# Performance work log

Measured on AMD Instinct MI355X. Metric: run time of the kernel, lower is better.

Reference implementation:

```python
import jax, jax.numpy as jnp
import numpy as np

D_IN = 1024
D_OUT = 1024
NUM_HEADS = 16
HEAD_DIM = D_OUT // NUM_HEADS


def setup_inputs() -> dict:
    key = jax.random.key(0)
    k_x, k_q, k_k, k_v, k_o = jax.random.split(key, 5)
    # Xavier-uniform-ish init for weights (stored as [d_in, d_out] for x @ W)
    lim = float(np.sqrt(6.0 / (D_IN + D_OUT)) / np.sqrt(2.0))
    lim_o = float(np.sqrt(6.0 / (D_OUT + D_OUT)))
    return {
        "x": jax.random.normal(k_x, (2, 2048, D_IN), dtype=jnp.float32),
        "W_query": jax.random.uniform(k_q, (D_IN, D_OUT), jnp.float32, -lim, lim),
        "W_key": jax.random.uniform(k_k, (D_IN, D_OUT), jnp.float32, -lim, lim),
        "W_value": jax.random.uniform(k_v, (D_IN, D_OUT), jnp.float32, -lim, lim),
        "W_out": jax.random.uniform(k_o, (D_OUT, D_OUT), jnp.float32, -lim_o, lim_o),
        "b_out": jnp.zeros((D_OUT,), dtype=jnp.float32),
    }


def reference(x, W_query, W_key, W_value, W_out, b_out):
    B, S, _ = x.shape
    scale = 1.0 / np.sqrt(HEAD_DIM)

    def split_heads(t):  # [B,S,D] -> [B,H,S,hd]
        return t.reshape(B, S, NUM_HEADS, HEAD_DIM).transpose(0, 2, 1, 3)

    q = split_heads(x @ W_query)
    k = split_heads(x @ W_key)
    v = split_heads(x @ W_value)

    scores = jnp.einsum("bhqd,bhkd->bhqk", q, k) * scale  # [B,H,S,S]
    causal = jnp.tril(jnp.ones((S, S), dtype=bool))  # True = keep
    scores = jnp.where(causal, scores, -jnp.inf)
    weights = jax.nn.softmax(scores, axis=-1)
    ctx = jnp.einsum("bhqk,bhkd->bhqd", weights, v)
    ctx = ctx.transpose(0, 2, 1, 3).reshape(B, S, D_OUT)
    return ctx @ W_out + b_out
```

## Files before the change

### kernel.cpp

```cpp
#include <hip/hip_runtime.h>
#include <hip/hip_bf16.h>


typedef __bf16 bf16_t;
typedef __bf16 bf16x4 __attribute__((ext_vector_type(4)));
typedef __bf16 bf16x8 __attribute__((ext_vector_type(8)));
typedef float f32x4 __attribute__((ext_vector_type(4)));

#define AS_GLOBAL __attribute__((address_space(1)))
#define AS_LDS    __attribute__((address_space(3)))

__device__ __forceinline__ void barrier_lgkm() {
    asm volatile("s_waitcnt lgkmcnt(0)\n\ts_barrier" ::: "memory");
}

__device__ __forceinline__ bf16x8 cvt_bf8(float4 lo, float4 hi) {
    bf16x8 r;
    r[0] = (bf16_t)lo.x; r[1] = (bf16_t)lo.y; r[2] = (bf16_t)lo.z; r[3] = (bf16_t)lo.w;
    r[4] = (bf16_t)hi.x; r[5] = (bf16_t)hi.y; r[6] = (bf16_t)hi.z; r[7] = (bf16_t)hi.w;
    return r;
}

__global__ __launch_bounds__(256) void transpose_cvt4(
    const float* __restrict__ W0, const float* __restrict__ W1,
    const float* __restrict__ W2, const float* __restrict__ W3,
    bf16_t* __restrict__ outbase) {
    __shared__ bf16_t T[64][65];
    int t = threadIdx.x;
    int k0 = blockIdx.x * 64, n0 = blockIdx.y * 64, z = blockIdx.z;
    const float* W = (z == 0) ? W0 : (z == 1) ? W1 : (z == 2) ? W2 : W3;
    bf16_t* WT = outbase + (size_t)z * 1048576;
#pragma unroll
    for (int c = 0; c < 4; c++) {
        int idx = c * 256 + t;
        int row = idx >> 4;
        int col4 = (idx & 15) * 4;
        float4 v = *(const float4*)(W + (k0 + row) * 1024 + n0 + col4);
        T[row][col4 + 0] = (bf16_t)v.x;
        T[row][col4 + 1] = (bf16_t)v.y;
        T[row][col4 + 2] = (bf16_t)v.z;
        T[row][col4 + 3] = (bf16_t)v.w;
    }
    __syncthreads();
#pragma unroll
    for (int c = 0; c < 4; c++) {
        int idx = c * 256 + t;
        int nrow = idx >> 4;
        int kc4 = (idx & 15) * 4;
        bf16x4 o;
        o[0] = T[kc4 + 0][nrow];
        o[1] = T[kc4 + 1][nrow];
        o[2] = T[kc4 + 2][nrow];
        o[3] = T[kc4 + 3][nrow];
        *(bf16x4*)(WT + (n0 + nrow) * 1024 + k0 + kc4) = o;
    }
}

__global__ __launch_bounds__(256) void qkv_gemm(
    const float* __restrict__ X,
    const bf16_t* __restrict__ WqT, const bf16_t* __restrict__ WkT,
    const bf16_t* __restrict__ WvT,
    bf16_t* __restrict__ Qo, bf16_t* __restrict__ Ko, bf16_t* __restrict__ Vo) {
    const int KD = 1024;
    __shared__ __align__(16) bf16_t As[2][4096];
    __shared__ __align__(16) bf16_t Bs[2][4096];
    int tid = threadIdx.x;
    int wave = tid >> 6, lane = tid & 63;
    int quad = lane >> 4, l16 = lane & 15;
    int wm = wave >> 1, wn = wave & 1;
    int z = blockIdx.z;
    const bf16_t* BT = (z == 0) ? WqT : (z == 1) ? WkT : WvT;
    int m0 = blockIdx.x * 128;
    int n0 = blockIdx.y * 128;

    int r = tid >> 2;
    int c8 = (((tid & 3) ^ ((tid >> 3) & 3))) * 8;
    const float*  gA0 = X + (size_t)(m0 + r) * KD + c8;
    const float*  gA1 = X + (size_t)(m0 + 64 + r) * KD + c8;
    const bf16_t* gB0 = BT + (size_t)(n0 + r) * KD + c8;
    const bf16_t* gB1 = BT + (size_t)(n0 + 64 + r) * KD + c8;

    f32x4 acc[4][4];
#pragma unroll
    for (int i = 0; i < 4; i++)
#pragma unroll
        for (int j = 0; j < 4; j++) acc[i][j] = (f32x4){0.f, 0.f, 0.f, 0.f};

    float4 fa0l = *(const float4*)gA0, fa0h = *(const float4*)(gA0 + 4);
    float4 fa1l = *(const float4*)gA1, fa1h = *(const float4*)(gA1 + 4);
    int4 sb0 = *(const int4*)gB0, sb1 = *(const int4*)gB1;
    *(bf16x8*)(As[0] + tid * 8) = cvt_bf8(fa0l, fa0h);
    *(bf16x8*)(As[0] + 2048 + tid * 8) = cvt_bf8(fa1l, fa1h);
    *(int4*)(Bs[0] + tid * 8) = sb0;
    *(int4*)(Bs[0] + 2048 + tid * 8) = sb1;
    fa0l = *(const float4*)(gA0 + 32); fa0h = *(const float4*)(gA0 + 36);
    fa1l = *(const float4*)(gA1 + 32); fa1h = *(const float4*)(gA1 + 36);
    sb0 = *(const int4*)(gB0 + 32); sb1 = *(const int4*)(gB1 + 32);

    int csw = (quad ^ ((l16 >> 1) & 3)) * 8;
#pragma unroll 1
    for (int kk = 0; kk < 32; kk += 2) {
        barrier_lgkm();
        bf16x8 af[4], bfr[4];
#pragma unroll
        for (int mt = 0; mt < 4; mt++)
            af[mt] = *(const bf16x8*)(As[0] + (wm * 64 + mt * 16 + l16) * 32 + csw);
#pragma unroll
        for (int nt = 0; nt < 4; nt++)
            bfr[nt] = *(const bf16x8*)(Bs[0] + (wn * 64 + nt * 16 + l16) * 32 + csw);
        *(bf16x8*)(As[1] + tid * 8) = cvt_bf8(fa0l, fa0h);
        *(bf16x8*)(As[1] + 2048 + tid * 8) = cvt_bf8(fa1l, fa1h);
        *(int4*)(Bs[1] + tid * 8) = sb0;
        *(int4*)(Bs[1] + 2048 + tid * 8) = sb1;
        if (kk + 2 < 32) {
            int k0 = (kk + 2) * 32;
            fa0l = *(const float4*)(gA0 + k0); fa0h = *(const float4*)(gA0 + k0 + 4);
            fa1l = *(const float4*)(gA1 + k0); fa1h = *(const float4*)(gA1 + k0 + 4);
            sb0 = *(const int4*)(gB0 + k0); sb1 = *(const int4*)(gB1 + k0);
        }
        if (z == 2) {
#pragma unroll
            for (int mt = 0; mt < 4; mt++)
#pragma unroll
                for (int nt = 0; nt < 4; nt++)
                    acc[mt][nt] = __builtin_amdgcn_mfma_f32_16x16x32_bf16(
                        bfr[nt], af[mt], acc[mt][nt], 0, 0, 0);
        } else {
#pragma unroll
            for (int mt = 0; mt < 4; mt++)
#pragma unroll
                for (int nt = 0; nt < 4; nt++)
                    acc[mt][nt] = __builtin_amdgcn_mfma_f32_16x16x32_bf16(
                        af[mt], bfr[nt], acc[mt][nt], 0, 0, 0);
        }
        barrier_lgkm();
#pragma unroll
        for (int mt = 0; mt < 4; mt++)
            af[mt] = *(const bf16x8*)(As[1] + (wm * 64 + mt * 16 + l16) * 32 + csw);
#pragma unroll
        for (int nt = 0; nt < 4; nt++)
            bfr[nt] = *(const bf16x8*)(Bs[1] + (wn * 64 + nt * 16 + l16) * 32 + csw);
        if (kk + 2 < 32) {
            *(bf16x8*)(As[0] + tid * 8) = cvt_bf8(fa0l, fa0h);
            *(bf16x8*)(As[0] + 2048 + tid * 8) = cvt_bf8(fa1l, fa1h);
            *(int4*)(Bs[0] + tid * 8) = sb0;
            *(int4*)(Bs[0] + 2048 + tid * 8) = sb1;
            if (kk + 3 < 32) {
                int k0 = (kk + 3) * 32;
                fa0l = *(const float4*)(gA0 + k0); fa0h = *(const float4*)(gA0 + k0 + 4);
                fa1l = *(const float4*)(gA1 + k0); fa1h = *(const float4*)(gA1 + k0 + 4);
                sb0 = *(const int4*)(gB0 + k0); sb1 = *(const int4*)(gB1 + k0);
            }
        }
        if (z == 2) {
#pragma unroll
            for (int mt = 0; mt < 4; mt++)
#pragma unroll
                for (int nt = 0; nt < 4; nt++)
                    acc[mt][nt] = __builtin_amdgcn_mfma_f32_16x16x32_bf16(
                        bfr[nt], af[mt], acc[mt][nt], 0, 0, 0);
        } else {
#pragma unroll
            for (int mt = 0; mt < 4; mt++)
#pragma unroll
                for (int nt = 0; nt < 4; nt++)
                    acc[mt][nt] = __builtin_amdgcn_mfma_f32_16x16x32_bf16(
                        af[mt], bfr[nt], acc[mt][nt], 0, 0, 0);
        }
    }

    if (z == 0) {
#pragma unroll
        for (int mt = 0; mt < 4; mt++) {
            int mg_base = m0 + wm * 64 + mt * 16 + quad * 4;
#pragma unroll
            for (int nt = 0; nt < 4; nt++) {
                int ng = n0 + wn * 64 + nt * 16 + l16;
                int h = ng >> 6, d = ng & 63;
#pragma unroll
                for (int rr = 0; rr < 4; rr++) {
                    int mg = mg_base + rr;
                    int b = mg >> 11, s = mg & 2047;
                    Qo[(((size_t)(b * 16 + h) * 2048) + s) * 64 + d] =
                        (bf16_t)acc[mt][nt][rr];
                }
            }
        }
    } else if (z == 1) {
#pragma unroll
        for (int mt = 0; mt < 4; mt++) {
            int mg_base = m0 + wm * 64 + mt * 16 + quad * 4;
#pragma unroll
            for (int nt = 0; nt < 4; nt++) {
                int ng = n0 + wn * 64 + nt * 16 + l16;
                int h = ng >> 6, dd = ng & 63;
#pragma unroll
                for (int rr = 0; rr < 4; rr++) {
                    int mg = mg_base + rr;
                    int b = mg >> 11, sl = mg & 2047;
                    int kt = sl >> 6, row = sl & 63;
                    int cc = (dd >> 3) ^ (row & 7);
                    Ko[(size_t)(b * 16 + h) * 131072 + kt * 4096 + row * 64 +
                       cc * 8 + (dd & 7)] = (bf16_t)acc[mt][nt][rr];
                }
            }
        }
    } else {
#pragma unroll
        for (int mt = 0; mt < 4; mt++) {
            int sg = m0 + wm * 64 + mt * 16 + l16;
            int b = sg >> 11, sl = sg & 2047;
            int kt = sl >> 6, srow = sl & 63;
#pragma unroll
            for (int nt = 0; nt < 4; nt++) {
                int dg_base = n0 + wn * 64 + nt * 16 + quad * 4;
#pragma unroll
                for (int rr = 0; rr < 4; rr++) {
                    int dg = dg_base + rr;
                    int h = dg >> 6, dd = dg & 63;
                    int cc = (srow >> 3) ^ (dd & 7);
                    Vo[(size_t)(b * 16 + h) * 131072 + kt * 4096 + dd * 64 +
                       cc * 8 + (srow & 7)] = (bf16_t)acc[mt][nt][rr];
                }
            }
        }
    }
}

__device__ __forceinline__ float exp_pwrite(f32x4 sc[4], bf16_t* Ps,
                                            int wave, int quad, int l16) {
    float part = 0.f;
    int rowbase = (wave * 16 + l16) * 64;
    int gran = (quad & 1) * 4;
    int chi = quad >> 1;
#pragma unroll
    for (int nt = 0; nt < 4; nt++) {
        f32x4 p;
#pragma unroll
        for (int rr = 0; rr < 4; rr++) {
            p[rr] = __builtin_amdgcn_exp2f(sc[nt][rr]);
            part += p[rr];
        }
        bf16x4 pb;
#pragma unroll
        for (int rr = 0; rr < 4; rr++) pb[rr] = (bf16_t)p[rr];
        int cc = (nt * 2 + chi) ^ (l16 & 7);
        *(bf16x4*)(Ps + rowbase + cc * 8 + gran) = pb;
    }
    part += __shfl_xor(part, 16);
    part += __shfl_xor(part, 32);
    return part;
}

__global__ __launch_bounds__(256) void attn(
    const bf16_t* __restrict__ Q, const bf16_t* __restrict__ Kt,
    const bf16_t* __restrict__ Vt, bf16_t* __restrict__ ctx) {
    const int S = 2048;
    __shared__ __align__(16) bf16_t Ks[2][4096];
    __shared__ __align__(16) bf16_t Vs[2][4096];
    __shared__ __align__(16) bf16_t Ps[2][4096];
    int tid = threadIdx.x, wave = tid >> 6, lane = tid & 63;
    int quad = lane >> 4, l16 = lane & 15;

    int f = blockIdx.x + 32 * blockIdx.y;
    int g = f >> 8, s = f & 255;
    int qtj = g ? (15 - (s & 15)) : (s & 15);
    int bh = (s >> 4) + 16 * g;
    int h = bh & 15, b = bh >> 4;
    int q0 = qtj * 128;

    const bf16_t* Qbh = Q + (size_t)bh * S * 64;
    const bf16_t* Kbh = Kt + (size_t)bh * 131072;
    const bf16_t* Vbh = Vt + (size_t)bh * 131072;

    const float qs = 0.125f * 1.44269504f;
    bf16x8 aQ[2][2];
#pragma unroll
    for (int sub = 0; sub < 2; sub++) {
        const bf16_t* rq = Qbh + (size_t)(q0 + sub * 64 + wave * 16 + l16) * 64;
#pragma unroll
        for (int ks = 0; ks < 2; ks++) {
            bf16x8 t = *(const bf16x8*)(rq + ks * 32 + quad * 8);
#pragma unroll
            for (int j = 0; j < 8; j++) t[j] = (bf16_t)((float)t[j] * qs);
            aQ[sub][ks] = t;
        }
    }

    float L[2] = {0.f, 0.f};
    f32x4 O[2][4];
#pragma unroll
    for (int sub = 0; sub < 2; sub++)
#pragma unroll
        for (int i = 0; i < 4; i++) O[sub][i] = (f32x4){0.f, 0.f, 0.f, 0.f};

    int tmax = 2 * qtj + 2;
    int4 ska = *(const int4*)(Kbh + tid * 8);
    int4 skb = *(const int4*)(Kbh + 2048 + tid * 8);
    int4 sva = *(const int4*)(Vbh + tid * 8);
    int4 svb = *(const int4*)(Vbh + 2048 + tid * 8);
    *(int4*)(Ks[0] + tid * 8) = ska; *(int4*)(Ks[0] + 2048 + tid * 8) = skb;
    *(int4*)(Vs[0] + tid * 8) = sva; *(int4*)(Vs[0] + 2048 + tid * 8) = svb;
    ska = *(const int4*)(Kbh + 4096 + tid * 8);
    skb = *(const int4*)(Kbh + 6144 + tid * 8);
    sva = *(const int4*)(Vbh + 4096 + tid * 8);
    svb = *(const int4*)(Vbh + 6144 + tid * 8);

#pragma unroll 1
    for (int kt = 0; kt < tmax; kt++) {
        int cur = kt & 1;
        barrier_lgkm();
        bf16x8 kf[4][2], vf[4][2];
#pragma unroll
        for (int nt = 0; nt < 4; nt++) {
            const bf16_t* krow = Ks[cur] + (nt * 16 + l16) * 64;
            const bf16_t* vrow = Vs[cur] + (nt * 16 + l16) * 64;
#pragma unroll
            for (int ks = 0; ks < 2; ks++) {
                int csw = ((ks * 4 + quad) ^ (l16 & 7)) * 8;
                kf[nt][ks] = *(const bf16x8*)(krow + csw);
                vf[nt][ks] = *(const bf16x8*)(vrow + csw);
            }
        }
        if (kt + 1 < tmax) {
            *(int4*)(Ks[cur ^ 1] + tid * 8) = ska;
            *(int4*)(Ks[cur ^ 1] + 2048 + tid * 8) = skb;
            *(int4*)(Vs[cur ^ 1] + tid * 8) = sva;
            *(int4*)(Vs[cur ^ 1] + 2048 + tid * 8) = svb;
        }
        if (kt + 2 < tmax) {
            const bf16_t* kg = Kbh + (kt + 2) * 4096;
            const bf16_t* vg = Vbh + (kt + 2) * 4096;
            ska = *(const int4*)(kg + tid * 8);
            skb = *(const int4*)(kg + 2048 + tid * 8);
            sva = *(const int4*)(vg + tid * 8);
            svb = *(const int4*)(vg + 2048 + tid * 8);
        }

        bool do_lo = (kt < tmax - 1);
        if (do_lo) {
            f32x4 sc[4];
#pragma unroll
            for (int nt = 0; nt < 4; nt++) {
                f32x4 ss = (f32x4){0.f, 0.f, 0.f, 0.f};
                ss = __builtin_amdgcn_mfma_f32_16x16x32_bf16(kf[nt][0], aQ[0][0], ss, 0, 0, 0);
                ss = __builtin_amdgcn_mfma_f32_16x16x32_bf16(kf[nt][1], aQ[0][1], ss, 0, 0, 0);
                sc[nt] = ss;
            }
            if (kt == tmax - 2) {
                int qg = q0 + wave * 16 + l16;
#pragma unroll
                for (int nt = 0; nt < 4; nt++)
#pragma unroll
                    for (int rr = 0; rr < 4; rr++)
                        if (kt * 64 + nt * 16 + quad * 4 + rr > qg) sc[nt][rr] = -1e30f;
            }
            L[0] += exp_pwrite(sc, Ps[0], wave, quad, l16);
        }
        {
            f32x4 sc[4];
#pragma unroll
            for (int nt = 0; nt < 4; nt++) {
                f32x4 ss = (f32x4){0.f, 0.f, 0.f, 0.f};
                ss = __builtin_amdgcn_mfma_f32_16x16x32_bf16(kf[nt][0], aQ[1][0], ss, 0, 0, 0);
                ss = __builtin_amdgcn_mfma_f32_16x16x32_bf16(kf[nt][1], aQ[1][1], ss, 0, 0, 0);
                sc[nt] = ss;
            }
            if (kt == tmax - 1) {
                int qg = q0 + 64 + wave * 16 + l16;
#pragma unroll
                for (int nt = 0; nt < 4; nt++)
#pragma unroll
                    for (int rr = 0; rr < 4; rr++)
                        if (kt * 64 + nt * 16 + quad * 4 + rr > qg) sc[nt][rr] = -1e30f;
            }
            L[1] += exp_pwrite(sc, Ps[1], wave, quad, l16);
        }

#pragma unroll
        for (int ks = 0; ks < 2; ks++) {
            int csw = ((ks * 4 + quad) ^ (l16 & 7)) * 8;
            bf16x8 aPhi = *(const bf16x8*)(Ps[1] + (wave * 16 + l16) * 64 + csw);
            bf16x8 aPlo;
            if (do_lo) aPlo = *(const bf16x8*)(Ps[0] + (wave * 16 + l16) * 64 + csw);
#pragma unroll
            for (int nt = 0; nt < 4; nt++) {
                O[1][nt] = __builtin_amdgcn_mfma_f32_16x16x32_bf16(aPhi, vf[nt][ks],
                                                                   O[1][nt], 0, 0, 0);
                if (do_lo)
                    O[0][nt] = __builtin_amdgcn_mfma_f32_16x16x32_bf16(aPlo, vf[nt][ks],
                                                                       O[0][nt], 0, 0, 0);
            }
        }
    }

#pragma unroll
    for (int sub = 0; sub < 2; sub++) {
        float il[4];
#pragma unroll
        for (int rr = 0; rr < 4; rr++) il[rr] = 1.f / __shfl(L[sub], quad * 4 + rr);
#pragma unroll
        for (int nt = 0; nt < 4; nt++) {
#pragma unroll
            for (int rr = 0; rr < 4; rr++) {
                int qoff = q0 + sub * 64 + wave * 16 + quad * 4 + rr;
                int col = h * 64 + nt * 16 + l16;
                ctx[(size_t)(b * 2048 + qoff) * 1024 + col] =
                    (bf16_t)(O[sub][nt][rr] * il[rr]);
            }
        }
    }
}

__global__ __launch_bounds__(256) void out_gemm(
    const bf16_t* __restrict__ A, const bf16_t* __restrict__ BT,
    const float* __restrict__ bias, float* __restrict__ Cout) {
    const int KD = 1024;
    __shared__ __align__(16) bf16_t As[2][2048];
    __shared__ __align__(16) bf16_t Bs[2][4096];
    int tid = threadIdx.x;
    int wave = tid >> 6, lane = tid & 63;
    int quad = lane >> 4, l16 = lane & 15;
    int wm = wave >> 1, wn = wave & 1;
    int m0 = blockIdx.x * 64;
    int n0 = blockIdx.y * 128;

    int r = tid >> 2;
    int c8 = (((tid & 3) ^ ((tid >> 3) & 3))) * 8;
    const bf16_t* gA  = A + (size_t)(m0 + r) * KD + c8;
    const bf16_t* gB0 = BT + (size_t)(n0 + r) * KD + c8;
    const bf16_t* gB1 = BT + (size_t)(n0 + 64 + r) * KD + c8;

    f32x4 acc[2][4];
#pragma unroll
    for (int i = 0; i < 2; i++)
#pragma unroll
        for (int j = 0; j < 4; j++) acc[i][j] = (f32x4){0.f, 0.f, 0.f, 0.f};

    int4 sa = *(const int4*)gA;
    int4 sb0 = *(const int4*)gB0, sb1 = *(const int4*)gB1;
    *(int4*)(As[0] + tid * 8) = sa;
    *(int4*)(Bs[0] + tid * 8) = sb0;
    *(int4*)(Bs[0] + 2048 + tid * 8) = sb1;
    sa = *(const int4*)(gA + 32);
    sb0 = *(const int4*)(gB0 + 32); sb1 = *(const int4*)(gB1 + 32);

    int csw = (quad ^ ((l16 >> 1) & 3)) * 8;
#pragma unroll 1
    for (int kk = 0; kk < 32; kk += 2) {
        barrier_lgkm();
        bf16x8 af[2], bfr[4];
#pragma unroll
        for (int mt = 0; mt < 2; mt++)
            af[mt] = *(const bf16x8*)(As[0] + (wm * 32 + mt * 16 + l16) * 32 + csw);
#pragma unroll
        for (int nt = 0; nt < 4; nt++)
            bfr[nt] = *(const bf16x8*)(Bs[0] + (wn * 64 + nt * 16 + l16) * 32 + csw);
        *(int4*)(As[1] + tid * 8) = sa;
        *(int4*)(Bs[1] + tid * 8) = sb0;
        *(int4*)(Bs[1] + 2048 + tid * 8) = sb1;
        if (kk + 2 < 32) {
            int k0 = (kk + 2) * 32;
            sa = *(const int4*)(gA + k0);
            sb0 = *(const int4*)(gB0 + k0); sb1 = *(const int4*)(gB1 + k0);
        }
#pragma unroll
        for (int mt = 0; mt < 2; mt++)
#pragma unroll
            for (int nt = 0; nt < 4; nt++)
                acc[mt][nt] = __builtin_amdgcn_mfma_f32_16x16x32_bf16(af[mt], bfr[nt],
                                                                      acc[mt][nt], 0, 0, 0);
        barrier_lgkm();
#pragma unroll
        for (int mt = 0; mt < 2; mt++)
            af[mt] = *(const bf16x8*)(As[1] + (wm * 32 + mt * 16 + l16) * 32 + csw);
#pragma unroll
        for (int nt = 0; nt < 4; nt++)
            bfr[nt] = *(const bf16x8*)(Bs[1] + (wn * 64 + nt * 16 + l16) * 32 + csw);
        if (kk + 2 < 32) {
            *(int4*)(As[0] + tid * 8) = sa;
            *(int4*)(Bs[0] + tid * 8) = sb0;
            *(int4*)(Bs[0] + 2048 + tid * 8) = sb1;
            if (kk + 3 < 32) {
                int k0 = (kk + 3) * 32;
                sa = *(const int4*)(gA + k0);
                sb0 = *(const int4*)(gB0 + k0); sb1 = *(const int4*)(gB1 + k0);
            }
        }
#pragma unroll
        for (int mt = 0; mt < 2; mt++)
#pragma unroll
            for (int nt = 0; nt < 4; nt++)
                acc[mt][nt] = __builtin_amdgcn_mfma_f32_16x16x32_bf16(af[mt], bfr[nt],
                                                                      acc[mt][nt], 0, 0, 0);
    }

#pragma unroll
    for (int mt = 0; mt < 2; mt++) {
        int mg_base = m0 + wm * 32 + mt * 16 + quad * 4;
#pragma unroll
        for (int nt = 0; nt < 4; nt++) {
            int ng = n0 + wn * 64 + nt * 16 + l16;
            float bv = bias[ng];
#pragma unroll
            for (int rr = 0; rr < 4; rr++) {
                int mg = mg_base + rr;
                Cout[(size_t)mg * 1024 + ng] = acc[mt][nt][rr] + bv;
            }
        }
    }
}

extern "C" void kernel_launch(void* const* d_in, const int* in_sizes, int n_in,
                              void* d_out, int out_size, void* d_ws, size_t ws_size,
                              hipStream_t stream) {
    const float* x  = (const float*)d_in[0];
    const float* Wq = (const float*)d_in[1];
    const float* Wk = (const float*)d_in[2];
    const float* Wv = (const float*)d_in[3];
    const float* Wo = (const float*)d_in[4];
    const float* bo = (const float*)d_in[5];
    float* out = (float*)d_out;
    char* ws = (char*)d_ws;

    bf16_t* WTs  = (bf16_t*)(ws + (8u << 20));
    bf16_t* WqT  = WTs;
    bf16_t* WkT  = WTs + 1048576;
    bf16_t* WvT  = WTs + 2097152;
    bf16_t* WoT  = WTs + 3145728;
    bf16_t* Qb   = (bf16_t*)(ws + (16u << 20));
    bf16_t* Kb   = (bf16_t*)(ws + (24u << 20));
    bf16_t* Vb   = (bf16_t*)(ws + (32u << 20));
    bf16_t* ctxb = (bf16_t*)(ws + (40u << 20));

    transpose_cvt4<<<dim3(16, 16, 4), 256, 0, stream>>>(Wq, Wk, Wv, Wo, WTs);
    qkv_gemm<<<dim3(32, 8, 3), 256, 0, stream>>>(x, WqT, WkT, WvT, Qb, Kb, Vb);
    attn<<<dim3(32, 16), 256, 0, stream>>>(Qb, Kb, Vb, ctxb);
    out_gemm<<<dim3(64, 8), 256, 0, stream>>>(ctxb, WoT, bo, out);
}
```

Baseline: 186.9 us.

## Fuse all stages into one cooperative persistent megakernel with grid syncs

```diff
diff --git a/kernel.cpp b/kernel.cpp
--- a/kernel.cpp
+++ b/kernel.cpp
@@ -1,27 +1,566 @@
 #include <hip/hip_runtime.h>
 #include <hip/hip_bf16.h>
-
+#include <hip/hip_cooperative_groups.h>
+
+
+namespace cg = cooperative_groups;
 
 typedef __bf16 bf16_t;
 typedef __bf16 bf16x4 __attribute__((ext_vector_type(4)));
 typedef __bf16 bf16x8 __attribute__((ext_vector_type(8)));
 typedef float f32x4 __attribute__((ext_vector_type(4)));
 
-#define AS_GLOBAL __attribute__((address_space(1)))
-#define AS_LDS    __attribute__((address_space(3)))
+__device__ int g_j1, g_j2;
 
 __device__ __forceinline__ void barrier_lgkm() {
     asm volatile("s_waitcnt lgkmcnt(0)\n\ts_barrier" ::: "memory");
 }
 
-__device__ __forceinline__ bf16x8 cvt_bf8(float4 lo, float4 hi) {
-    bf16x8 r;
-    r[0] = (bf16_t)lo.x; r[1] = (bf16_t)lo.y; r[2] = (bf16_t)lo.z; r[3] = (bf16_t)lo.w;
-    r[4] = (bf16_t)hi.x; r[5] = (bf16_t)hi.y; r[6] = (bf16_t)hi.z; r[7] = (bf16_t)hi.w;
-    return r;
-}
-
-__global__ __launch_bounds__(256) void transpose_cvt4(
+__device__ __forceinline__ float exp_pwrite(f32x4 sc[4], bf16_t* Ps,
+                                            int wave, int quad, int l16) {
+    float part = 0.f;
+    int rowbase = (wave * 16 + l16) * 64;
+    int gran = (quad & 1) * 4;
+    int chi = quad >> 1;
+#pragma unroll
+    for (int nt = 0; nt < 4; nt++) {
+        f32x4 p;
+#pragma unroll
+        for (int rr = 0; rr < 4; rr++) {
+            p[rr] = __builtin_amdgcn_exp2f(sc[nt][rr]);
+            part += p[rr];
+        }
+        bf16x4 pb;
+#pragma unroll
+        for (int rr = 0; rr < 4; rr++) pb[rr] = (bf16_t)p[rr];
+        int cc = (nt * 2 + chi) ^ (l16 & 7);
+        *(bf16x4*)(Ps + rowbase + cc * 8 + gran) = pb;
+    }
+    part += __shfl_xor(part, 16);
+    part += __shfl_xor(part, 32);
+    return part;
+}
+
+
+__device__ __forceinline__ void qkv_body(
+    int mb, int nb, int z, const bf16_t* xb, const bf16_t* WqT,
+    const bf16_t* WkT, const bf16_t* WvT, bf16_t* Qb, bf16_t* Kb, bf16_t* Vb,
+    bf16_t* As, bf16_t* Bs, int tid, int wave, int quad, int l16) {
+    const int KD = 1024;
+    const bf16_t* BT = (z == 0) ? WqT : (z == 1) ? WkT : WvT;
+    int m0 = mb * 128, n0 = nb * 128;
+    int wm = wave >> 1, wn = wave & 1;
+    int r = tid >> 2;
+    int c8 = (((tid & 3) ^ ((tid >> 3) & 3))) * 8;
+    const bf16_t* gA0 = xb + (size_t)(m0 + r) * KD + c8;
+    const bf16_t* gA1 = xb + (size_t)(m0 + 64 + r) * KD + c8;
+    const bf16_t* gB0 = BT + (size_t)(n0 + r) * KD + c8;
+    const bf16_t* gB1 = BT + (size_t)(n0 + 64 + r) * KD + c8;
+
+    f32x4 acc[4][4];
+#pragma unroll
+    for (int i = 0; i < 4; i++)
+#pragma unroll
+        for (int j = 0; j < 4; j++) acc[i][j] = (f32x4){0.f, 0.f, 0.f, 0.f};
+
+    int4 sa0 = *(const int4*)gA0, sa1 = *(const int4*)gA1;
+    int4 sb0 = *(const int4*)gB0, sb1 = *(const int4*)gB1;
+    *(int4*)(As + tid * 8) = sa0;
+    *(int4*)(As + 2048 + tid * 8) = sa1;
+    *(int4*)(Bs + tid * 8) = sb0;
+    *(int4*)(Bs + 2048 + tid * 8) = sb1;
+    sa0 = *(const int4*)(gA0 + 32); sa1 = *(const int4*)(gA1 + 32);
+    sb0 = *(const int4*)(gB0 + 32); sb1 = *(const int4*)(gB1 + 32);
+
+    int csw = (quad ^ ((l16 >> 1) & 3)) * 8;
+#pragma unroll 1
+    for (int kk = 0; kk < 32; kk += 2) {
+        barrier_lgkm();
+        bf16x8 af[4], bfr[4];
+#pragma unroll
+        for (int mt = 0; mt < 4; mt++)
+            af[mt] = *(const bf16x8*)(As + (wm * 64 + mt * 16 + l16) * 32 + csw);
+#pragma unroll
+        for (int nt = 0; nt < 4; nt++)
+            bfr[nt] = *(const bf16x8*)(Bs + (wn * 64 + nt * 16 + l16) * 32 + csw);
+        *(int4*)(As + 4096 + tid * 8) = sa0;
+        *(int4*)(As + 6144 + tid * 8) = sa1;
+        *(int4*)(Bs + 4096 + tid * 8) = sb0;
+        *(int4*)(Bs + 6144 + tid * 8) = sb1;
+        if (kk + 2 < 32) {
+            int k0 = (kk + 2) * 32;
+            sa0 = *(const int4*)(gA0 + k0); sa1 = *(const int4*)(gA1 + k0);
+            sb0 = *(const int4*)(gB0 + k0); sb1 = *(const int4*)(gB1 + k0);
+        }
+        if (z == 2) {
+#pragma unroll
+            for (int mt = 0; mt < 4; mt++)
+#pragma unroll
+                for (int nt = 0; nt < 4; nt++)
+                    acc[mt][nt] = __builtin_amdgcn_mfma_f32_16x16x32_bf16(
+                        bfr[nt], af[mt], acc[mt][nt], 0, 0, 0);
+        } else {
+#pragma unroll
+            for (int mt = 0; mt < 4; mt++)
+#pragma unroll
+                for (int nt = 0; nt < 4; nt++)
+                    acc[mt][nt] = __builtin_amdgcn_mfma_f32_16x16x32_bf16(
+                        af[mt], bfr[nt], acc[mt][nt], 0, 0, 0);
+        }
+        barrier_lgkm();
+#pragma unroll
+        for (int mt = 0; mt < 4; mt++)
+            af[mt] = *(const bf16x8*)(As + 4096 + (wm * 64 + mt * 16 + l16) * 32 + csw);
+#pragma unroll
+        for (int nt = 0; nt < 4; nt++)
+            bfr[nt] = *(const bf16x8*)(Bs + 4096 + (wn * 64 + nt * 16 + l16) * 32 + csw);
+        if (kk + 2 < 32) {
+            *(int4*)(As + tid * 8) = sa0;
+            *(int4*)(As + 2048 + tid * 8) = sa1;
+            *(int4*)(Bs + tid * 8) = sb0;
+            *(int4*)(Bs + 2048 + tid * 8) = sb1;
+            if (kk + 3 < 32) {
+                int k0 = (kk + 3) * 32;
+                sa0 = *(const int4*)(gA0 + k0); sa1 = *(const int4*)(gA1 + k0);
+                sb0 = *(const int4*)(gB0 + k0); sb1 = *(const int4*)(gB1 + k0);
+            }
+        }
+        if (z == 2) {
+#pragma unroll
+            for (int mt = 0; mt < 4; mt++)
+#pragma unroll
+                for (int nt = 0; nt < 4; nt++)
+                    acc[mt][nt] = __builtin_amdgcn_mfma_f32_16x16x32_bf16(
+                        bfr[nt], af[mt], acc[mt][nt], 0, 0, 0);
+        } else {
+#pragma unroll
+            for (int mt = 0; mt < 4; mt++)
+#pragma unroll
+                for (int nt = 0; nt < 4; nt++)
+                    acc[mt][nt] = __builtin_amdgcn_mfma_f32_16x16x32_bf16(
+                        af[mt], bfr[nt], acc[mt][nt], 0, 0, 0);
+        }
+    }
+
+    if (z == 0) {
+#pragma unroll
+        for (int mt = 0; mt < 4; mt++) {
+            int mg_base = m0 + (wave >> 1) * 64 + mt * 16 + quad * 4;
+#pragma unroll
+            for (int nt = 0; nt < 4; nt++) {
+                int ng = n0 + (wave & 1) * 64 + nt * 16 + l16;
+                int h = ng >> 6, d = ng & 63;
+#pragma unroll
+                for (int rr = 0; rr < 4; rr++) {
+                    int mg = mg_base + rr;
+                    int b = mg >> 11, s = mg & 2047;
+                    Qb[(((size_t)(b * 16 + h) * 2048) + s) * 64 + d] =
+                        (bf16_t)acc[mt][nt][rr];
+                }
+            }
+        }
+    } else if (z == 1) {
+#pragma unroll
+        for (int mt = 0; mt < 4; mt++) {
+            int mg_base = m0 + (wave >> 1) * 64 + mt * 16 + quad * 4;
+#pragma unroll
+            for (int nt = 0; nt < 4; nt++) {
+                int ng = n0 + (wave & 1) * 64 + nt * 16 + l16;
+                int h = ng >> 6, dd = ng & 63;
+#pragma unroll
+                for (int rr = 0; rr < 4; rr++) {
+                    int mg = mg_base + rr;
+                    int b = mg >> 11, sl = mg & 2047;
+                    int kt = sl >> 6, row = sl & 63;
+                    int cc = (dd >> 3) ^ (row & 7);
+                    Kb[(size_t)(b * 16 + h) * 131072 + kt * 4096 + row * 64 +
+                       cc * 8 + (dd & 7)] = (bf16_t)acc[mt][nt][rr];
+                }
+            }
+        }
+    } else {
+#pragma unroll
+        for (int mt = 0; mt < 4; mt++) {
+            int sg = m0 + (wave >> 1) * 64 + mt * 16 + l16;
+            int b = sg >> 11, sl = sg & 2047;
+            int kt = sl >> 6, srow = sl & 63;
+#pragma unroll
+            for (int nt = 0; nt < 4; nt++) {
+                int dg_base = n0 + (wave & 1) * 64 + nt * 16 + quad * 4;
+#pragma unroll
+                for (int rr = 0; rr < 4; rr++) {
+                    int dg = dg_base + rr;
+                    int h = dg >> 6, dd = dg & 63;
+                    int cc = (srow >> 3) ^ (dd & 7);
+                    Vb[(size_t)(b * 16 + h) * 131072 + kt * 4096 + dd * 64 +
+                       cc * 8 + (srow & 7)] = (bf16_t)acc[mt][nt][rr];
+                }
+            }
+        }
+    }
+}
+
+__device__ __forceinline__ void attn_body(
+    int qtj, int bh, const bf16_t* Qb, const bf16_t* Kb, const bf16_t* Vb,
+    bf16_t* ctxb, bf16_t* Ks, bf16_t* Vs, bf16_t* Ps,
+    int tid, int wave, int quad, int l16) {
+    int h = bh & 15, b = bh >> 4;
+    int q0 = qtj * 128;
+    const bf16_t* Qbh = Qb + (size_t)bh * 131072;
+    const bf16_t* Kbh = Kb + (size_t)bh * 131072;
+    const bf16_t* Vbh = Vb + (size_t)bh * 131072;
+
+    const float qs = 0.125f * 1.44269504f;
+    bf16x8 aQ[2][2];
+#pragma unroll
+    for (int sub = 0; sub < 2; sub++) {
+        const bf16_t* rq = Qbh + (size_t)(q0 + sub * 64 + wave * 16 + l16) * 64;
+#pragma unroll
+        for (int ks = 0; ks < 2; ks++) {
+            bf16x8 t = *(const bf16x8*)(rq + ks * 32 + quad * 8);
+#pragma unroll
+            for (int j = 0; j < 8; j++) t[j] = (bf16_t)((float)t[j] * qs);
+            aQ[sub][ks] = t;
+        }
+    }
+
+    float L[2] = {0.f, 0.f};
+    f32x4 O[2][4];
+#pragma unroll
+    for (int sub = 0; sub < 2; sub++)
+#pragma unroll
+        for (int i = 0; i < 4; i++) O[sub][i] = (f32x4){0.f, 0.f, 0.f, 0.f};
+
+    int tmax = 2 * qtj + 2;
+    int4 ska = *(const int4*)(Kbh + tid * 8);
+    int4 skb = *(const int4*)(Kbh + 2048 + tid * 8);
+    int4 sva = *(const int4*)(Vbh + tid * 8);
+    int4 svb = *(const int4*)(Vbh + 2048 + tid * 8);
+    *(int4*)(Ks + tid * 8) = ska; *(int4*)(Ks + 2048 + tid * 8) = skb;
+    *(int4*)(Vs + tid * 8) = sva; *(int4*)(Vs + 2048 + tid * 8) = svb;
+    ska = *(const int4*)(Kbh + 4096 + tid * 8);
+    skb = *(const int4*)(Kbh + 6144 + tid * 8);
+    sva = *(const int4*)(Vbh + 4096 + tid * 8);
+    svb = *(const int4*)(Vbh + 6144 + tid * 8);
+
+#pragma unroll 1
+    for (int kt = 0; kt < tmax; kt++) {
+        int cur = (kt & 1) * 4096;
+        barrier_lgkm();
+        bf16x8 kf[4][2], vf[4][2];
+#pragma unroll
+        for (int nt = 0; nt < 4; nt++) {
+            const bf16_t* krow = Ks + cur + (nt * 16 + l16) * 64;
+            const bf16_t* vrow = Vs + cur + (nt * 16 + l16) * 64;
+#pragma unroll
+            for (int ks = 0; ks < 2; ks++) {
+                int csw = ((ks * 4 + quad) ^ (l16 & 7)) * 8;
+                kf[nt][ks] = *(const bf16x8*)(krow + csw);
+                vf[nt][ks] = *(const bf16x8*)(vrow + csw);
+            }
+        }
+        if (kt + 1 < tmax) {
+            int nxt = cur ^ 4096;
+            *(int4*)(Ks + nxt + tid * 8) = ska;
+            *(int4*)(Ks + nxt + 2048 + tid * 8) = skb;
+            *(int4*)(Vs + nxt + tid * 8) = sva;
+            *(int4*)(Vs + nxt + 2048 + tid * 8) = svb;
+        }
+        if (kt + 2 < tmax) {
+            const bf16_t* kg = Kbh + (kt + 2) * 4096;
+            const bf16_t* vg = Vbh + (kt + 2) * 4096;
+            ska = *(const int4*)(kg + tid * 8);
+            skb = *(const int4*)(kg + 2048 + tid * 8);
+            sva = *(const int4*)(vg + tid * 8);
+            svb = *(const int4*)(vg + 2048 + tid * 8);
+        }
+
+        bool do_lo = (kt < tmax - 1);
+        if (do_lo) {
+            f32x4 sc[4];
+#pragma unroll
+            for (int nt = 0; nt < 4; nt++) {
+                f32x4 ss = (f32x4){0.f, 0.f, 0.f, 0.f};
+                ss = __builtin_amdgcn_mfma_f32_16x16x32_bf16(kf[nt][0], aQ[0][0], ss, 0, 0, 0);
+                ss = __builtin_amdgcn_mfma_f32_16x16x32_bf16(kf[nt][1], aQ[0][1], ss, 0, 0, 0);
+                sc[nt] = ss;
+            }
+            if (kt == tmax - 2) {
+                int qg = q0 + wave * 16 + l16;
+#pragma unroll
+                for (int nt = 0; nt < 4; nt++)
+#pragma unroll
+                    for (int rr = 0; rr < 4; rr++)
+                        if (kt * 64 + nt * 16 + quad * 4 + rr > qg) sc[nt][rr] = -1e30f;
+            }
+            L[0] += exp_pwrite(sc, Ps, wave, quad, l16);
+        }
+        {
+            f32x4 sc[4];
+#pragma unroll
+            for (int nt = 0; nt < 4; nt++) {
+                f32x4 ss = (f32x4){0.f, 0.f, 0.f, 0.f};
+                ss = __builtin_amdgcn_mfma_f32_16x16x32_bf16(kf[nt][0], aQ[1][0], ss, 0, 0, 0);
+                ss = __builtin_amdgcn_mfma_f32_16x16x32_bf16(kf[nt][1], aQ[1][1], ss, 0, 0, 0);
+                sc[nt] = ss;
+            }
+            if (kt == tmax - 1) {
+                int qg = q0 + 64 + wave * 16 + l16;
+#pragma unroll
+                for (int nt = 0; nt < 4; nt++)
+#pragma unroll
+                    for (int rr = 0; rr < 4; rr++)
+                        if (kt * 64 + nt * 16 + quad * 4 + rr > qg) sc[nt][rr] = -1e30f;
+            }
+            L[1] += exp_pwrite(sc, Ps + 4096, wave, quad, l16);
+        }
+
+#pragma unroll
+        for (int ks = 0; ks < 2; ks++) {
+            int csw = ((ks * 4 + quad) ^ (l16 & 7)) * 8;
+            bf16x8 aPhi = *(const bf16x8*)(Ps + 4096 + (wave * 16 + l16) * 64 + csw);
+            bf16x8 aPlo;
+            if (do_lo) aPlo = *(const bf16x8*)(Ps + (wave * 16 + l16) * 64 + csw);
+#pragma unroll
+            for (int nt = 0; nt < 4; nt++) {
+                O[1][nt] = __builtin_amdgcn_mfma_f32_16x16x32_bf16(aPhi, vf[nt][ks],
+                                                                   O[1][nt], 0, 0, 0);
+                if (do_lo)
+                    O[0][nt] = __builtin_amdgcn_mfma_f32_16x16x32_bf16(aPlo, vf[nt][ks],
+                                                                       O[0][nt], 0, 0, 0);
+            }
+        }
+    }
+
+#pragma unroll
+    for (int sub = 0; sub < 2; sub++) {
+        float il[4];
+#pragma unroll
+        for (int rr = 0; rr < 4; rr++) il[rr] = 1.f / __shfl(L[sub], quad * 4 + rr);
+#pragma unroll
+        for (int nt = 0; nt < 4; nt++) {
+#pragma unroll
+            for (int rr = 0; rr < 4; rr++) {
+                int qoff = q0 + sub * 64 + wave * 16 + quad * 4 + rr;
+                int col = h * 64 + nt * 16 + l16;
+                ctxb[(size_t)(b * 2048 + qoff) * 1024 + col] =
+                    (bf16_t)(O[sub][nt][rr] * il[rr]);
+            }
+        }
+    }
+}
+
+__device__ __forceinline__ void out_body(
+    int m0, int n0, const bf16_t* ctxb, const bf16_t* WoT, const float* bo,
+    float* out, bf16_t* As, bf16_t* Bs, int tid, int wave, int quad, int l16) {
+    const int KD = 1024;
+    int wm = wave >> 1, wn = wave & 1;
+    int r = tid >> 2;
+    int c8 = (((tid & 3) ^ ((tid >> 3) & 3))) * 8;
+    const bf16_t* gA  = ctxb + (size_t)(m0 + r) * KD + c8;
+    const bf16_t* gB0 = WoT + (size_t)(n0 + r) * KD + c8;
+    const bf16_t* gB1 = WoT + (size_t)(n0 + 64 + r) * KD + c8;
+
+    f32x4 acc[2][4];
+#pragma unroll
+    for (int i = 0; i < 2; i++)
+#pragma unroll
+        for (int j = 0; j < 4; j++) acc[i][j] = (f32x4){0.f, 0.f, 0.f, 0.f};
+
+    int4 sa = *(const int4*)gA;
+    int4 sb0 = *(const int4*)gB0, sb1 = *(const int4*)gB1;
+    *(int4*)(As + tid * 8) = sa;
+    *(int4*)(Bs + tid * 8) = sb0;
+    *(int4*)(Bs + 2048 + tid * 8) = sb1;
+    sa = *(const int4*)(gA + 32);
+    sb0 = *(const int4*)(gB0 + 32); sb1 = *(const int4*)(gB1 + 32);
+
+    int csw = (quad ^ ((l16 >> 1) & 3)) * 8;
+#pragma unroll 1
+    for (int kk = 0; kk < 32; kk += 2) {
+        barrier_lgkm();
+        bf16x8 af[2], bfr[4];
+#pragma unroll
+        for (int mt = 0; mt < 2; mt++)
+            af[mt] = *(const bf16x8*)(As + (wm * 32 + mt * 16 + l16) * 32 + csw);
+#pragma unroll
+        for (int nt = 0; nt < 4; nt++)
+            bfr[nt] = *(const bf16x8*)(Bs + (wn * 64 + nt * 16 + l16) * 32 + csw);
+        *(int4*)(As + 2048 + tid * 8) = sa;
+        *(int4*)(Bs + 4096 + tid * 8) = sb0;
+        *(int4*)(Bs + 6144 + tid * 8) = sb1;
+        if (kk + 2 < 32) {
+            int k0 = (kk + 2) * 32;
+            sa = *(const int4*)(gA + k0);
+            sb0 = *(const int4*)(gB0 + k0); sb1 = *(const int4*)(gB1 + k0);
+        }
+#pragma unroll
+        for (int mt = 0; mt < 2; mt++)
+#pragma unroll
+            for (int nt = 0; nt < 4; nt++)
+                acc[mt][nt] = __builtin_amdgcn_mfma_f32_16x16x32_bf16(
+                    af[mt], bfr[nt], acc[mt][nt], 0, 0, 0);
+        barrier_lgkm();
+#pragma unroll
+        for (int mt = 0; mt < 2; mt++)
+            af[mt] = *(const bf16x8*)(As + 2048 + (wm * 32 + mt * 16 + l16) * 32 + csw);
+#pragma unroll
+        for (int nt = 0; nt < 4; nt++)
+            bfr[nt] = *(const bf16x8*)(Bs + 4096 + (wn * 64 + nt * 16 + l16) * 32 + csw);
+        if (kk + 2 < 32) {
+            *(int4*)(As + tid * 8) = sa;
+            *(int4*)(Bs + tid * 8) = sb0;
+            *(int4*)(Bs + 2048 + tid * 8) = sb1;
+            if (kk + 3 < 32) {
+                int k0 = (kk + 3) * 32;
+                sa = *(const int4*)(gA + k0);
+                sb0 = *(const int4*)(gB0 + k0); sb1 = *(const int4*)(gB1 + k0);
+            }
+        }
+#pragma unroll
+        for (int mt = 0; mt < 2; mt++)
+#pragma unroll
+            for (int nt = 0; nt < 4; nt++)
+                acc[mt][nt] = __builtin_amdgcn_mfma_f32_16x16x32_bf16(
+                    af[mt], bfr[nt], acc[mt][nt], 0, 0, 0);
+    }
+
+#pragma unroll
+    for (int mt = 0; mt < 2; mt++) {
+        int mg_base = m0 + wm * 32 + mt * 16 + quad * 4;
+#pragma unroll
+        for (int nt = 0; nt < 4; nt++) {
+            int ng = n0 + wn * 64 + nt * 16 + l16;
+            float bv = bo[ng];
+#pragma unroll
+            for (int rr = 0; rr < 4; rr++) {
+                int mg = mg_base + rr;
+                out[(size_t)mg * 1024 + ng] = acc[mt][nt][rr] + bv;
+            }
+        }
+    }
+}
+
+__global__ __launch_bounds__(256, 2) void mega(
+    const float* __restrict__ x, const float* __restrict__ Wq,
+    const float* __restrict__ Wk, const float* __restrict__ Wv,
+    const float* __restrict__ Wo, const float* __restrict__ bo,
+    float* __restrict__ out, char* __restrict__ ws) {
+    __shared__ __align__(16) char smem[49152];
+    __shared__ int s_job;
+    cg::grid_group grid = cg::this_grid();
+
+    int tid = threadIdx.x;
+    int wave = tid >> 6, lane = tid & 63;
+    int quad = lane >> 4, l16 = lane & 15;
+    int blk = blockIdx.x;
+
+    bf16_t* xb   = (bf16_t*)ws;
+    bf16_t* WTs  = (bf16_t*)(ws + (8u << 20));
+    bf16_t* Qb   = (bf16_t*)(ws + (16u << 20));
+    bf16_t* Kb   = (bf16_t*)(ws + (24u << 20));
+    bf16_t* Vb   = (bf16_t*)(ws + (32u << 20));
+    bf16_t* ctxb = (bf16_t*)(ws + (40u << 20));
+
+    if (blk == 0 && tid == 0) { g_j1 = 0; g_j2 = 0; }
+    {
+        const float4* x4 = (const float4*)x;
+        bf16x4* xb4 = (bf16x4*)xb;
+#pragma unroll 1
+        for (int i = blk * 256 + tid; i < 1048576; i += 512 * 256) {
+            float4 v = x4[i];
+            bf16x4 o;
+            o[0] = (bf16_t)v.x; o[1] = (bf16_t)v.y;
+            o[2] = (bf16_t)v.z; o[3] = (bf16_t)v.w;
+            xb4[i] = o;
+        }
+        bf16_t* T = (bf16_t*)smem;
+#pragma unroll 1
+        for (int jj = blk; jj < 1024; jj += 512) {
+            int k0 = (jj & 15) * 64, n0 = ((jj >> 4) & 15) * 64, z = jj >> 8;
+            const float* W = (z == 0) ? Wq : (z == 1) ? Wk : (z == 2) ? Wv : Wo;
+            bf16_t* WT = WTs + (size_t)z * 1048576;
+            __syncthreads();
+#pragma unroll
+            for (int c = 0; c < 4; c++) {
+                int idx = c * 256 + tid;
+                int row = idx >> 4, col4 = (idx & 15) * 4;
+                float4 v = *(const float4*)(W + (k0 + row) * 1024 + n0 + col4);
+                T[row * 65 + col4 + 0] = (bf16_t)v.x;
+                T[row * 65 + col4 + 1] = (bf16_t)v.y;
+                T[row * 65 + col4 + 2] = (bf16_t)v.z;
+                T[row * 65 + col4 + 3] = (bf16_t)v.w;
+            }
+            __syncthreads();
+#pragma unroll
+            for (int c = 0; c < 4; c++) {
+                int idx = c * 256 + tid;
+                int nrow = idx >> 4, kc4 = (idx & 15) * 4;
+                bf16x4 o;
+                o[0] = T[(kc4 + 0) * 65 + nrow];
+                o[1] = T[(kc4 + 1) * 65 + nrow];
+                o[2] = T[(kc4 + 2) * 65 + nrow];
+                o[3] = T[(kc4 + 3) * 65 + nrow];
+                *(bf16x4*)(WT + (n0 + nrow) * 1024 + k0 + kc4) = o;
+            }
+        }
+    }
+    __threadfence();
+    grid.sync();
+
+    {
+        bf16_t* As = (bf16_t*)smem;
+        bf16_t* Bs = (bf16_t*)(smem + 16384);
+#pragma unroll 1
+        while (true) {
+            __syncthreads();
+            if (tid == 0) s_job = atomicAdd(&g_j1, 1);
+            __syncthreads();
+            int j = s_job;
+            if (j >= 768) break;
+            qkv_body(j & 31, (j >> 5) & 7, j >> 8, xb, WTs, WTs + 1048576,
+                     WTs + 2097152, Qb, Kb, Vb, As, Bs, tid, wave, quad, l16);
+        }
+    }
+    __threadfence();
+    grid.sync();
+
+    {
+        bf16_t* Ks = (bf16_t*)smem;
+        bf16_t* Vs = (bf16_t*)(smem + 16384);
+        bf16_t* Ps = (bf16_t*)(smem + 32768);
+#pragma unroll 1
+        while (true) {
+            __syncthreads();
+            if (tid == 0) s_job = atomicAdd(&g_j2, 1);
+            __syncthreads();
+            int j = s_job;
+            if (j >= 512) break;
+            attn_body(15 - (j >> 5), j & 31, Qb, Kb, Vb, ctxb,
+                      Ks, Vs, Ps, tid, wave, quad, l16);
+        }
+    }
+    __threadfence();
+    grid.sync();
+
+    {
+        bf16_t* As = (bf16_t*)smem;
+        bf16_t* Bs = (bf16_t*)(smem + 8192);
+        out_body((blk & 63) * 64, (blk >> 6) * 128, ctxb, WTs + 3145728, bo,
+                 out, As, Bs, tid, wave, quad, l16);
+    }
+}
+
+__global__ __launch_bounds__(256) void cvt_k(const float* __restrict__ src,
+                                             bf16_t* __restrict__ dst) {
+    int i = blockIdx.x * 256 + threadIdx.x;
+    float4 v = ((const float4*)src)[i];
+    bf16x4 o;
+    o[0] = (bf16_t)v.x; o[1] = (bf16_t)v.y; o[2] = (bf16_t)v.z; o[3] = (bf16_t)v.w;
+    ((bf16x4*)dst)[i] = o;
+}
+
+__global__ __launch_bounds__(256) void transpose_k(
     const float* __restrict__ W0, const float* __restrict__ W1,
     const float* __restrict__ W2, const float* __restrict__ W3,
     bf16_t* __restrict__ outbase) {
@@ -33,8 +572,7 @@
 #pragma unroll
     for (int c = 0; c < 4; c++) {
         int idx = c * 256 + t;
-        int row = idx >> 4;
-        int col4 = (idx & 15) * 4;
+        int row = idx >> 4, col4 = (idx & 15) * 4;
         float4 v = *(const float4*)(W + (k0 + row) * 1024 + n0 + col4);
         T[row][col4 + 0] = (bf16_t)v.x;
         T[row][col4 + 1] = (bf16_t)v.y;
@@ -45,8 +583,7 @@
 #pragma unroll
     for (int c = 0; c < 4; c++) {
         int idx = c * 256 + t;
-        int nrow = idx >> 4;
-        int kc4 = (idx & 15) * 4;
+        int nrow = idx >> 4, kc4 = (idx & 15) * 4;
         bf16x4 o;
         o[0] = T[kc4 + 0][nrow];
         o[1] = T[kc4 + 1][nrow];
@@ -56,459 +593,40 @@
     }
 }
 
-__global__ __launch_bounds__(256) void qkv_gemm(
-    const float* __restrict__ X,
-    const bf16_t* __restrict__ WqT, const bf16_t* __restrict__ WkT,
-    const bf16_t* __restrict__ WvT,
-    bf16_t* __restrict__ Qo, bf16_t* __restrict__ Ko, bf16_t* __restrict__ Vo) {
-    const int KD = 1024;
+__global__ __launch_bounds__(256) void qkv_k(
+    const bf16_t* __restrict__ xb, const bf16_t* __restrict__ WTs,
+    bf16_t* __restrict__ Qb, bf16_t* __restrict__ Kb, bf16_t* __restrict__ Vb) {
     __shared__ __align__(16) bf16_t As[2][4096];
     __shared__ __align__(16) bf16_t Bs[2][4096];
-    int tid = threadIdx.x;
-    int wave = tid >> 6, lane = tid & 63;
-    int quad = lane >> 4, l16 = lane & 15;
-    int wm = wave >> 1, wn = wave & 1;
-    int z = blockIdx.z;
-    const bf16_t* BT = (z == 0) ? WqT : (z == 1) ? WkT : WvT;
-    int m0 = blockIdx.x * 128;
-    int n0 = blockIdx.y * 128;
-
-    int r = tid >> 2;
-    int c8 = (((tid & 3) ^ ((tid >> 3) & 3))) * 8;
-    const float*  gA0 = X + (size_t)(m0 + r) * KD + c8;
-    const float*  gA1 = X + (size_t)(m0 + 64 + r) * KD + c8;
-    const bf16_t* gB0 = BT + (size_t)(n0 + r) * KD + c8;
-    const bf16_t* gB1 = BT + (size_t)(n0 + 64 + r) * KD + c8;
-
-    f32x4 acc[4][4];
-#pragma unroll
-    for (int i = 0; i < 4; i++)
-#pragma unroll
-        for (int j = 0; j < 4; j++) acc[i][j] = (f32x4){0.f, 0.f, 0.f, 0.f};
-
-    float4 fa0l = *(const float4*)gA0, fa0h = *(const float4*)(gA0 + 4);
-    float4 fa1l = *(const float4*)gA1, fa1h = *(const float4*)(gA1 + 4);
-    int4 sb0 = *(const int4*)gB0, sb1 = *(const int4*)gB1;
-    *(bf16x8*)(As[0] + tid * 8) = cvt_bf8(fa0l, fa0h);
-    *(bf16x8*)(As[0] + 2048 + tid * 8) = cvt_bf8(fa1l, fa1h);
-    *(int4*)(Bs[0] + tid * 8) = sb0;
-    *(int4*)(Bs[0] + 2048 + tid * 8) = sb1;
-    fa0l = *(const float4*)(gA0 + 32); fa0h = *(const float4*)(gA0 + 36);
-    fa1l = *(const float4*)(gA1 + 32); fa1h = *(const float4*)(gA1 + 36);
-    sb0 = *(const int4*)(gB0 + 32); sb1 = *(const int4*)(gB1 + 32);
-
-    int csw = (quad ^ ((l16 >> 1) & 3)) * 8;
-#pragma unroll 1
-    for (int kk = 0; kk < 32; kk += 2) {
-        barrier_lgkm();
-        bf16x8 af[4], bfr[4];
-#pragma unroll
-        for (int mt = 0; mt < 4; mt++)
-            af[mt] = *(const bf16x8*)(As[0] + (wm * 64 + mt * 16 + l16) * 32 + csw);
-#pragma unroll
-        for (int nt = 0; nt < 4; nt++)
-            bfr[nt] = *(const bf16x8*)(Bs[0] + (wn * 64 + nt * 16 + l16) * 32 + csw);
-        *(bf16x8*)(As[1] + tid * 8) = cvt_bf8(fa0l, fa0h);
-        *(bf16x8*)(As[1] + 2048 + tid * 8) = cvt_bf8(fa1l, fa1h);
-        *(int4*)(Bs[1] + tid * 8) = sb0;
-        *(int4*)(Bs[1] + 2048 + tid * 8) = sb1;
-        if (kk + 2 < 32) {
-            int k0 = (kk + 2) * 32;
-            fa0l = *(const float4*)(gA0 + k0); fa0h = *(const float4*)(gA0 + k0 + 4);
-            fa1l = *(const float4*)(gA1 + k0); fa1h = *(const float4*)(gA1 + k0 + 4);
-            sb0 = *(const int4*)(gB0 + k0); sb1 = *(const int4*)(gB1 + k0);
-        }
-        if (z == 2) {
-#pragma unroll
-            for (int mt = 0; mt < 4; mt++)
-#pragma unroll
-                for (int nt = 0; nt < 4; nt++)
-                    acc[mt][nt] = __builtin_amdgcn_mfma_f32_16x16x32_bf16(
-                        bfr[nt], af[mt], acc[mt][nt], 0, 0, 0);
-        } else {
-#pragma unroll
-            for (int mt = 0; mt < 4; mt++)
-#pragma unroll
-                for (int nt = 0; nt < 4; nt++)
-                    acc[mt][nt] = __builtin_amdgcn_mfma_f32_16x16x32_bf16(
-                        af[mt], bfr[nt], acc[mt][nt], 0, 0, 0);
-        }
-        barrier_lgkm();
-#pragma unroll
-        for (int mt = 0; mt < 4; mt++)
-            af[mt] = *(const bf16x8*)(As[1] + (wm * 64 + mt * 16 + l16) * 32 + csw);
-#pragma unroll
-        for (int nt = 0; nt < 4; nt++)
-            bfr[nt] = *(const bf16x8*)(Bs[1] + (wn * 64 + nt * 16 + l16) * 32 + csw);
-        if (kk + 2 < 32) {
-            *(bf16x8*)(As[0] + tid * 8) = cvt_bf8(fa0l, fa0h);
-            *(bf16x8*)(As[0] + 2048 + tid * 8) = cvt_bf8(fa1l, fa1h);
-            *(int4*)(Bs[0] + tid * 8) = sb0;
-            *(int4*)(Bs[0] + 2048 + tid * 8) = sb1;
-            if (kk + 3 < 32) {
-                int k0 = (kk + 3) * 32;
-                fa0l = *(const float4*)(gA0 + k0); fa0h = *(const float4*)(gA0 + k0 + 4);
-                fa1l = *(const float4*)(gA1 + k0); fa1h = *(const float4*)(gA1 + k0 + 4);
-                sb0 = *(const int4*)(gB0 + k0); sb1 = *(const int4*)(gB1 + k0);
-            }
-        }
-        if (z == 2) {
-#pragma unroll
-            for (int mt = 0; mt < 4; mt++)
-#pragma unroll
-                for (int nt = 0; nt < 4; nt++)
-                    acc[mt][nt] = __builtin_amdgcn_mfma_f32_16x16x32_bf16(
-                        bfr[nt], af[mt], acc[mt][nt], 0, 0, 0);
-        } else {
-#pragma unroll
-            for (int mt = 0; mt < 4; mt++)
-#pragma unroll
-                for (int nt = 0; nt < 4; nt++)
-                    acc[mt][nt] = __builtin_amdgcn_mfma_f32_16x16x32_bf16(
-                        af[mt], bfr[nt], acc[mt][nt], 0, 0, 0);
-        }
-    }
-
-    if (z == 0) {
-#pragma unroll
-        for (int mt = 0; mt < 4; mt++) {
-            int mg_base = m0 + wm * 64 + mt * 16 + quad * 4;
-#pragma unroll
-            for (int nt = 0; nt < 4; nt++) {
-                int ng = n0 + wn * 64 + nt * 16 + l16;
-                int h = ng >> 6, d = ng & 63;
-#pragma unroll
-                for (int rr = 0; rr < 4; rr++) {
-                    int mg = mg_base + rr;
-                    int b = mg >> 11, s = mg & 2047;
-                    Qo[(((size_t)(b * 16 + h) * 2048) + s) * 64 + d] =
-                        (bf16_t)acc[mt][nt][rr];
-                }
-            }
-        }
-    } else if (z == 1) {
-#pragma unroll
-        for (int mt = 0; mt < 4; mt++) {
-            int mg_base = m0 + wm * 64 + mt * 16 + quad * 4;
-#pragma unroll
-            for (int nt = 0; nt < 4; nt++) {
-                int ng = n0 + wn * 64 + nt * 16 + l16;
-                int h = ng >> 6, dd = ng & 63;
-#pragma unroll
-                for (int rr = 0; rr < 4; rr++) {
-                    int mg = mg_base + rr;
-                    int b = mg >> 11, sl = mg & 2047;
-                    int kt = sl >> 6, row = sl & 63;
-                    int cc = (dd >> 3) ^ (row & 7);
-                    Ko[(size_t)(b * 16 + h) * 131072 + kt * 4096 + row * 64 +
-                       cc * 8 + (dd & 7)] = (bf16_t)acc[mt][nt][rr];
-                }
-            }
-        }
-    } else {
-#pragma unroll
-        for (int mt = 0; mt < 4; mt++) {
-            int sg = m0 + wm * 64 + mt * 16 + l16;
-            int b = sg >> 11, sl = sg & 2047;
-            int kt = sl >> 6, srow = sl & 63;
-#pragma unroll
-            for (int nt = 0; nt < 4; nt++) {
-                int dg_base = n0 + wn * 64 + nt * 16 + quad * 4;
-#pragma unroll
-                for (int rr = 0; rr < 4; rr++) {
-                    int dg = dg_base + rr;
-                    int h = dg >> 6, dd = dg & 63;
-                    int cc = (srow >> 3) ^ (dd & 7);
-                    Vo[(size_t)(b * 16 + h) * 131072 + kt * 4096 + dd * 64 +
-                       cc * 8 + (srow & 7)] = (bf16_t)acc[mt][nt][rr];
-                }
-            }
-        }
-    }
-}
-
-__device__ __forceinline__ float exp_pwrite(f32x4 sc[4], bf16_t* Ps,
-                                            int wave, int quad, int l16) {
-    float part = 0.f;
-    int rowbase = (wave * 16 + l16) * 64;
-    int gran = (quad & 1) * 4;
-    int chi = quad >> 1;
-#pragma unroll
-    for (int nt = 0; nt < 4; nt++) {
-        f32x4 p;
-#pragma unroll
-        for (int rr = 0; rr < 4; rr++) {
-            p[rr] = __builtin_amdgcn_exp2f(sc[nt][rr]);
-            part += p[rr];
-        }
-        bf16x4 pb;
-#pragma unroll
-        for (int rr = 0; rr < 4; rr++) pb[rr] = (bf16_t)p[rr];
-        int cc = (nt * 2 + chi) ^ (l16 & 7);
-        *(bf16x4*)(Ps + rowbase + cc * 8 + gran) = pb;
-    }
-    part += __shfl_xor(part, 16);
-    part += __shfl_xor(part, 32);
-    return part;
-}
-
-__global__ __launch_bounds__(256) void attn(
-    const bf16_t* __restrict__ Q, const bf16_t* __restrict__ Kt,
-    const bf16_t* __restrict__ Vt, bf16_t* __restrict__ ctx) {
-    const int S = 2048;
+    int tid = threadIdx.x, wave = tid >> 6, lane = tid & 63;
+    qkv_body(blockIdx.x, blockIdx.y, blockIdx.z, xb, WTs, WTs + 1048576,
+             WTs + 2097152, Qb, Kb, Vb, As[0], Bs[0], tid, wave,
+             lane >> 4, lane & 15);
+}
+
+__global__ __launch_bounds__(256) void attn_k(
+    const bf16_t* __restrict__ Qb, const bf16_t* __restrict__ Kb,
+    const bf16_t* __restrict__ Vb, bf16_t* __restrict__ ctxb) {
     __shared__ __align__(16) bf16_t Ks[2][4096];
     __shared__ __align__(16) bf16_t Vs[2][4096];
     __shared__ __align__(16) bf16_t Ps[2][4096];
     int tid = threadIdx.x, wave = tid >> 6, lane = tid & 63;
-    int quad = lane >> 4, l16 = lane & 15;
-
     int f = blockIdx.x + 32 * blockIdx.y;
     int g = f >> 8, s = f & 255;
     int qtj = g ? (15 - (s & 15)) : (s & 15);
     int bh = (s >> 4) + 16 * g;
-    int h = bh & 15, b = bh >> 4;
-    int q0 = qtj * 128;
-
-    const bf16_t* Qbh = Q + (size_t)bh * S * 64;
-    const bf16_t* Kbh = Kt + (size_t)bh * 131072;
-    const bf16_t* Vbh = Vt + (size_t)bh * 131072;
-
-    const float qs = 0.125f * 1.44269504f;
-    bf16x8 aQ[2][2];
-#pragma unroll
-    for (int sub = 0; sub < 2; sub++) {
-        const bf16_t* rq = Qbh + (size_t)(q0 + sub * 64 + wave * 16 + l16) * 64;
-#pragma unroll
-        for (int ks = 0; ks < 2; ks++) {
-            bf16x8 t = *(const bf16x8*)(rq + ks * 32 + quad * 8);
-#pragma unroll
-            for (int j = 0; j < 8; j++) t[j] = (bf16_t)((float)t[j] * qs);
-            aQ[sub][ks] = t;
-        }
-    }
-
-    float L[2] = {0.f, 0.f};
-    f32x4 O[2][4];
-#pragma unroll
-    for (int sub = 0; sub < 2; sub++)
-#pragma unroll
-        for (int i = 0; i < 4; i++) O[sub][i] = (f32x4){0.f, 0.f, 0.f, 0.f};
-
-    int tmax = 2 * qtj + 2;
-    int4 ska = *(const int4*)(Kbh + tid * 8);
-    int4 skb = *(const int4*)(Kbh + 2048 + tid * 8);
-    int4 sva = *(const int4*)(Vbh + tid * 8);
-    int4 svb = *(const int4*)(Vbh + 2048 + tid * 8);
-    *(int4*)(Ks[0] + tid * 8) = ska; *(int4*)(Ks[0] + 2048 + tid * 8) = skb;
-    *(int4*)(Vs[0] + tid * 8) = sva; *(int4*)(Vs[0] + 2048 + tid * 8) = svb;
-    ska = *(const int4*)(Kbh + 4096 + tid * 8);
-    skb = *(const int4*)(Kbh + 6144 + tid * 8);
-    sva = *(const int4*)(Vbh + 4096 + tid * 8);
-    svb = *(const int4*)(Vbh + 6144 + tid * 8);
-
-#pragma unroll 1
-    for (int kt = 0; kt < tmax; kt++) {
-        int cur = kt & 1;
-        barrier_lgkm();
-        bf16x8 kf[4][2], vf[4][2];
-#pragma unroll
-        for (int nt = 0; nt < 4; nt++) {
-            const bf16_t* krow = Ks[cur] + (nt * 16 + l16) * 64;
-            const bf16_t* vrow = Vs[cur] + (nt * 16 + l16) * 64;
-#pragma unroll
-            for (int ks = 0; ks < 2; ks++) {
-                int csw = ((ks * 4 + quad) ^ (l16 & 7)) * 8;
-                kf[nt][ks] = *(const bf16x8*)(krow + csw);
-                vf[nt][ks] = *(const bf16x8*)(vrow + csw);
-            }
-        }
-        if (kt + 1 < tmax) {
-            *(int4*)(Ks[cur ^ 1] + tid * 8) = ska;
-            *(int4*)(Ks[cur ^ 1] + 2048 + tid * 8) = skb;
-            *(int4*)(Vs[cur ^ 1] + tid * 8) = sva;
-            *(int4*)(Vs[cur ^ 1] + 2048 + tid * 8) = svb;
-        }
-        if (kt + 2 < tmax) {
-            const bf16_t* kg = Kbh + (kt + 2) * 4096;
-            const bf16_t* vg = Vbh + (kt + 2) * 4096;
-            ska = *(const int4*)(kg + tid * 8);
-            skb = *(const int4*)(kg + 2048 + tid * 8);
-            sva = *(const int4*)(vg + tid * 8);
-            svb = *(const int4*)(vg + 2048 + tid * 8);
-        }
-
-        bool do_lo = (kt < tmax - 1);
-        if (do_lo) {
-            f32x4 sc[4];
-#pragma unroll
-            for (int nt = 0; nt < 4; nt++) {
-                f32x4 ss = (f32x4){0.f, 0.f, 0.f, 0.f};
-                ss = __builtin_amdgcn_mfma_f32_16x16x32_bf16(kf[nt][0], aQ[0][0], ss, 0, 0, 0);
-                ss = __builtin_amdgcn_mfma_f32_16x16x32_bf16(kf[nt][1], aQ[0][1], ss, 0, 0, 0);
-                sc[nt] = ss;
-            }
-            if (kt == tmax - 2) {
-                int qg = q0 + wave * 16 + l16;
-#pragma unroll
-                for (int nt = 0; nt < 4; nt++)
-#pragma unroll
-                    for (int rr = 0; rr < 4; rr++)
-                        if (kt * 64 + nt * 16 + quad * 4 + rr > qg) sc[nt][rr] = -1e30f;
-            }
-            L[0] += exp_pwrite(sc, Ps[0], wave, quad, l16);
-        }
-        {
-            f32x4 sc[4];
-#pragma unroll
-            for (int nt = 0; nt < 4; nt++) {
-                f32x4 ss = (f32x4){0.f, 0.f, 0.f, 0.f};
-                ss = __builtin_amdgcn_mfma_f32_16x16x32_bf16(kf[nt][0], aQ[1][0], ss, 0, 0, 0);
-                ss = __builtin_amdgcn_mfma_f32_16x16x32_bf16(kf[nt][1], aQ[1][1], ss, 0, 0, 0);
-                sc[nt] = ss;
-            }
-            if (kt == tmax - 1) {
-                int qg = q0 + 64 + wave * 16 + l16;
-#pragma unroll
-                for (int nt = 0; nt < 4; nt++)
-#pragma unroll
-                    for (int rr = 0; rr < 4; rr++)
-                        if (kt * 64 + nt * 16 + quad * 4 + rr > qg) sc[nt][rr] = -1e30f;
-            }
-            L[1] += exp_pwrite(sc, Ps[1], wave, quad, l16);
-        }
-
-#pragma unroll
-        for (int ks = 0; ks < 2; ks++) {
-            int csw = ((ks * 4 + quad) ^ (l16 & 7)) * 8;
-            bf16x8 aPhi = *(const bf16x8*)(Ps[1] + (wave * 16 + l16) * 64 + csw);
-            bf16x8 aPlo;
-            if (do_lo) aPlo = *(const bf16x8*)(Ps[0] + (wave * 16 + l16) * 64 + csw);
-#pragma unroll
-            for (int nt = 0; nt < 4; nt++) {
-                O[1][nt] = __builtin_amdgcn_mfma_f32_16x16x32_bf16(aPhi, vf[nt][ks],
-                                                                   O[1][nt], 0, 0, 0);
-                if (do_lo)
-                    O[0][nt] = __builtin_amdgcn_mfma_f32_16x16x32_bf16(aPlo, vf[nt][ks],
-                                                                       O[0][nt], 0, 0, 0);
-            }
-        }
-    }
-
-#pragma unroll
-    for (int sub = 0; sub < 2; sub++) {
-        float il[4];
-#pragma unroll
-        for (int rr = 0; rr < 4; rr++) il[rr] = 1.f / __shfl(L[sub], quad * 4 + rr);
-#pragma unroll
-        for (int nt = 0; nt < 4; nt++) {
-#pragma unroll
-            for (int rr = 0; rr < 4; rr++) {
-                int qoff = q0 + sub * 64 + wave * 16 + quad * 4 + rr;
-                int col = h * 64 + nt * 16 + l16;
-                ctx[(size_t)(b * 2048 + qoff) * 1024 + col] =
-                    (bf16_t)(O[sub][nt][rr] * il[rr]);
-            }
-        }
-    }
-}
-
-__global__ __launch_bounds__(256) void out_gemm(
-    const bf16_t* __restrict__ A, const bf16_t* __restrict__ BT,
-    const float* __restrict__ bias, float* __restrict__ Cout) {
-    const int KD = 1024;
+    attn_body(qtj, bh, Qb, Kb, Vb, ctxb, Ks[0], Vs[0], Ps[0],
+              tid, wave, lane >> 4, lane & 15);
+}
+
+__global__ __launch_bounds__(256) void out_k(
+    const bf16_t* __restrict__ ctxb, const bf16_t* __restrict__ WoT,
+    const float* __restrict__ bo, float* __restrict__ out) {
     __shared__ __align__(16) bf16_t As[2][2048];
     __shared__ __align__(16) bf16_t Bs[2][4096];
-    int tid = threadIdx.x;
-    int wave = tid >> 6, lane = tid & 63;
-    int quad = lane >> 4, l16 = lane & 15;
-    int wm = wave >> 1, wn = wave & 1;
-    int m0 = blockIdx.x * 64;
-    int n0 = blockIdx.y * 128;
-
-    int r = tid >> 2;
-    int c8 = (((tid & 3) ^ ((tid >> 3) & 3))) * 8;
-    const bf16_t* gA  = A + (size_t)(m0 + r) * KD + c8;
-    const bf16_t* gB0 = BT + (size_t)(n0 + r) * KD + c8;
-    const bf16_t* gB1 = BT + (size_t)(n0 + 64 + r) * KD + c8;
-
-    f32x4 acc[2][4];
-#pragma unroll
-    for (int i = 0; i < 2; i++)
-#pragma unroll
-        for (int j = 0; j < 4; j++) acc[i][j] = (f32x4){0.f, 0.f, 0.f, 0.f};
-
-    int4 sa = *(const int4*)gA;
-    int4 sb0 = *(const int4*)gB0, sb1 = *(const int4*)gB1;
-    *(int4*)(As[0] + tid * 8) = sa;
-    *(int4*)(Bs[0] + tid * 8) = sb0;
-    *(int4*)(Bs[0] + 2048 + tid * 8) = sb1;
-    sa = *(const int4*)(gA + 32);
-    sb0 = *(const int4*)(gB0 + 32); sb1 = *(const int4*)(gB1 + 32);
-
-    int csw = (quad ^ ((l16 >> 1) & 3)) * 8;
-#pragma unroll 1
-    for (int kk = 0; kk < 32; kk += 2) {
-        barrier_lgkm();
-        bf16x8 af[2], bfr[4];
-#pragma unroll
-        for (int mt = 0; mt < 2; mt++)
-            af[mt] = *(const bf16x8*)(As[0] + (wm * 32 + mt * 16 + l16) * 32 + csw);
-#pragma unroll
-        for (int nt = 0; nt < 4; nt++)
-            bfr[nt] = *(const bf16x8*)(Bs[0] + (wn * 64 + nt * 16 + l16) * 32 + csw);
-        *(int4*)(As[1] + tid * 8) = sa;
-        *(int4*)(Bs[1] + tid * 8) = sb0;
-        *(int4*)(Bs[1] + 2048 + tid * 8) = sb1;
-        if (kk + 2 < 32) {
-            int k0 = (kk + 2) * 32;
-            sa = *(const int4*)(gA + k0);
-            sb0 = *(const int4*)(gB0 + k0); sb1 = *(const int4*)(gB1 + k0);
-        }
-#pragma unroll
-        for (int mt = 0; mt < 2; mt++)
-#pragma unroll
-            for (int nt = 0; nt < 4; nt++)
-                acc[mt][nt] = __builtin_amdgcn_mfma_f32_16x16x32_bf16(af[mt], bfr[nt],
-                                                                      acc[mt][nt], 0, 0, 0);
-        barrier_lgkm();
-#pragma unroll
-        for (int mt = 0; mt < 2; mt++)
-            af[mt] = *(const bf16x8*)(As[1] + (wm * 32 + mt * 16 + l16) * 32 + csw);
-#pragma unroll
-        for (int nt = 0; nt < 4; nt++)
-            bfr[nt] = *(const bf16x8*)(Bs[1] + (wn * 64 + nt * 16 + l16) * 32 + csw);
-        if (kk + 2 < 32) {
-            *(int4*)(As[0] + tid * 8) = sa;
-            *(int4*)(Bs[0] + tid * 8) = sb0;
-            *(int4*)(Bs[0] + 2048 + tid * 8) = sb1;
-            if (kk + 3 < 32) {
-                int k0 = (kk + 3) * 32;
-                sa = *(const int4*)(gA + k0);
-                sb0 = *(const int4*)(gB0 + k0); sb1 = *(const int4*)(gB1 + k0);
-            }
-        }
-#pragma unroll
-        for (int mt = 0; mt < 2; mt++)
-#pragma unroll
-            for (int nt = 0; nt < 4; nt++)
-                acc[mt][nt] = __builtin_amdgcn_mfma_f32_16x16x32_bf16(af[mt], bfr[nt],
-                                                                      acc[mt][nt], 0, 0, 0);
-    }
-
-#pragma unroll
-    for (int mt = 0; mt < 2; mt++) {
-        int mg_base = m0 + wm * 32 + mt * 16 + quad * 4;
-#pragma unroll
-        for (int nt = 0; nt < 4; nt++) {
-            int ng = n0 + wn * 64 + nt * 16 + l16;
-            float bv = bias[ng];
-#pragma unroll
-            for (int rr = 0; rr < 4; rr++) {
-                int mg = mg_base + rr;
-                Cout[(size_t)mg * 1024 + ng] = acc[mt][nt][rr] + bv;
-            }
-        }
-    }
+    int tid = threadIdx.x, wave = tid >> 6, lane = tid & 63;
+    out_body(blockIdx.x * 64, blockIdx.y * 128, ctxb, WoT, bo, out,
+             As[0], Bs[0], tid, wave, lane >> 4, lane & 15);
 }
 
 extern "C" void kernel_launch(void* const* d_in, const int* in_sizes, int n_in,
@@ -523,18 +641,21 @@
     float* out = (float*)d_out;
     char* ws = (char*)d_ws;
 
-    bf16_t* WTs  = (bf16_t*)(ws + (8u << 20));
-    bf16_t* WqT  = WTs;
-    bf16_t* WkT  = WTs + 1048576;
-    bf16_t* WvT  = WTs + 2097152;
-    bf16_t* WoT  = WTs + 3145728;
-    bf16_t* Qb   = (bf16_t*)(ws + (16u << 20));
-    bf16_t* Kb   = (bf16_t*)(ws + (24u << 20));
-    bf16_t* Vb   = (bf16_t*)(ws + (32u << 20));
-    bf16_t* ctxb = (bf16_t*)(ws + (40u << 20));
-
-    transpose_cvt4<<<dim3(16, 16, 4), 256, 0, stream>>>(Wq, Wk, Wv, Wo, WTs);
-    qkv_gemm<<<dim3(32, 8, 3), 256, 0, stream>>>(x, WqT, WkT, WvT, Qb, Kb, Vb);
-    attn<<<dim3(32, 16), 256, 0, stream>>>(Qb, Kb, Vb, ctxb);
-    out_gemm<<<dim3(64, 8), 256, 0, stream>>>(ctxb, WoT, bo, out);
-}
+    void* kargs[] = {(void*)&x, (void*)&Wq, (void*)&Wk, (void*)&Wv,
+                     (void*)&Wo, (void*)&bo, (void*)&out, (void*)&ws};
+    hipError_t err = hipLaunchCooperativeKernel((const void*)mega, dim3(512),
+                                                dim3(256), kargs, 0, stream);
+    if (err != hipSuccess) {
+        bf16_t* xb   = (bf16_t*)ws;
+        bf16_t* WTs  = (bf16_t*)(ws + (8u << 20));
+        bf16_t* Qb   = (bf16_t*)(ws + (16u << 20));
+        bf16_t* Kb   = (bf16_t*)(ws + (24u << 20));
+        bf16_t* Vb   = (bf16_t*)(ws + (32u << 20));
+        bf16_t* ctxb = (bf16_t*)(ws + (40u << 20));
+        cvt_k<<<4096, 256, 0, stream>>>(x, xb);
+        transpose_k<<<dim3(16, 16, 4), 256, 0, stream>>>(Wq, Wk, Wv, Wo, WTs);
+        qkv_k<<<dim3(32, 8, 3), 256, 0, stream>>>(xb, WTs, Qb, Kb, Vb);
+        attn_k<<<dim3(32, 16), 256, 0, stream>>>(Qb, Kb, Vb, ctxb);
+        out_k<<<dim3(64, 8), 256, 0, stream>>>(ctxb, WTs + 3145728, bo, out);
+    }
+}
```

New measurement: 584.6 us. +212.7%, slower.
